# Performance work log

Measured on AMD Instinct MI355X. Metric: run time of the kernel, lower is better.

## Reference

```python
import jax, jax.numpy as jnp
import numpy as np

E = 768; H = 64; W = 64; K = 3; PAD = 1
CH = [30, 100, 150, 220, 268]


def _conv3x3(x, w, b):
    out = jax.lax.conv_general_dilated(x, w, (1, 1), ((PAD, PAD), (PAD, PAD)),
                                       dimension_numbers=('NCHW', 'OIHW', 'NCHW'))
    return out + b[None, :, None, None]


def _deform_conv(x, offset, mask, w, b):
    # modulated deform_conv2d, group=1, stride=1, dil=1, pad=1 (torchvision semantics)
    N, C, Hh, Ww = x.shape
    KK = K * K
    off = offset.reshape(N, KK, 2, Hh, Ww)  # [...,0]=dy, [...,1]=dx per kernel tap
    ky = jnp.repeat(jnp.arange(K), K).astype(x.dtype)
    kx = jnp.tile(jnp.arange(K), K).astype(x.dtype)
    hg = jnp.arange(Hh, dtype=x.dtype)[None, None, :, None]
    wg = jnp.arange(Ww, dtype=x.dtype)[None, None, None, :]
    py = hg - PAD + ky[None, :, None, None] + off[:, :, 0]  # [N,9,H,W]
    px = wg - PAD + kx[None, :, None, None] + off[:, :, 1]
    y0 = jnp.floor(py); x0 = jnp.floor(px)
    xf = x.reshape(N, C, Hh * Ww)

    def gather(yi, xi):
        valid = ((yi >= 0) & (yi <= Hh - 1) & (xi >= 0) & (xi <= Ww - 1)).astype(x.dtype)
        yc = jnp.clip(yi, 0, Hh - 1).astype(jnp.int32)
        xc = jnp.clip(xi, 0, Ww - 1).astype(jnp.int32)
        idx = (yc * Ww + xc).reshape(N, 1, KK * Hh * Ww)
        g = jnp.take_along_axis(xf, idx, axis=2).reshape(N, C, KK, Hh, Ww)
        return g * valid[:, None]

    wy1 = py - y0; wx1 = px - x0; wy0 = 1.0 - wy1; wx0 = 1.0 - wx1
    samp = (gather(y0, x0) * (wy0 * wx0)[:, None]
            + gather(y0, x0 + 1) * (wy0 * wx1)[:, None]
            + gather(y0 + 1, x0) * (wy1 * wx0)[:, None]
            + gather(y0 + 1, x0 + 1) * (wy1 * wx1)[:, None])
    samp = samp * mask[:, None]  # modulation
    out = jnp.einsum('nckhw,ock->nohw', samp, w.reshape(w.shape[0], C, KK))
    return out + b[None, :, None, None]


def _block(x, conv_w, conv_b, off_w, off_b, msk_w, msk_b, bn_g, bn_b):
    # DefConv2d.forward: conv -> offset/mask linears -> deform conv -> BN(train stats) -> relu
    N, C, Hh, Ww = x.shape
    om = _conv3x3(x, conv_w, conv_b)
    om_hwc = om.transpose(0, 2, 3, 1)
    offset = (om_hwc @ off_w.T + off_b).transpose(0, 3, 1, 2)  # [N,18,H,W]
    mask = jax.nn.softmax(om_hwc @ msk_w.T + msk_b, axis=-1)   # [N,H,W,9]
    mask = mask.reshape(N, K * K, Hh, Ww)  # raw reshape, exactly as torch .reshape (no permute)
    out = _deform_conv(x, offset, mask, conv_w, conv_b)
    mu = out.mean(axis=(0, 2, 3), keepdims=True)
    var = out.var(axis=(0, 2, 3), keepdims=True)
    out = (out - mu) / jnp.sqrt(var + 1e-5) * bn_g[None, :, None, None] + bn_b[None, :, None, None]
    return jax.nn.relu(out)


def _cam(x, chq_w, chv_w, chz_w, ln_g, ln_b, spq_w, spv_w):
    xin = x
    N, C, Hh, Ww = x.shape  # N must be 1 (matches torch reshapes)
    # channel attention
    wv = jnp.einsum('nchw,oc->nohw', x, chv_w).reshape(C // 2, Hh * Ww)
    wq = jax.nn.softmax(jnp.einsum('nchw,oc->nohw', x, chq_w).reshape(Hh * Ww))
    wz = chz_w @ (wv @ wq)  # [C]
    wz = (wz - wz.mean()) / jnp.sqrt(wz.var() + 1e-5) * ln_g + ln_b
    x = jax.nn.sigmoid(wz)[None, :, None, None] * x
    # spatial attention
    wq = jax.nn.softmax(jnp.einsum('nchw,oc->nohw', x, spq_w).max(axis=(2, 3)).reshape(C // 2))
    wv = jnp.einsum('nchw,oc->nohw', x, spv_w).reshape(C // 2, Hh * Ww)
    wz = jax.nn.sigmoid(wq @ wv).reshape(1, 1, Hh, Ww)
    return wz * x + xin


def _forward(x1, x2, x3, x4, x5, conv_w, conv_b, off_w, off_b, msk_w, msk_b, bn_g, bn_b,
             chq_w, chv_w, chz_w, ln_g, ln_b, spq_w, spv_w,
             w1, w2, w3a, w3b, w4a, w4b, w5a, w5b, norm_g, norm_b):
    xper = [t.transpose(0, 3, 1, 2) for t in (x1, x2, x3, x4, x5)]
    blk = lambda t: _block(t, conv_w, conv_b, off_w, off_b, msk_w, msk_b, bn_g, bn_b)
    c1 = lambda t, w: jnp.einsum('nchw,oc->nohw', t, w)
    o1 = c1(blk(xper[0]), w1)
    o2 = c1(blk(xper[1]), w2)
    o3 = c1(blk(xper[2]), w3a) + c1(xper[2], w3b)
    o4 = c1(blk(xper[3]), w4a) + c1(xper[3], w4b)
    o5 = c1(blk(xper[4]), w5a) + c1(xper[4], w5b)
    out = jnp.concatenate((o1, o2, o3, o4, o5), axis=1)  # sum(CH)=768 channels
    out = _cam(out, chq_w, chv_w, chz_w, ln_g, ln_b, spq_w, spv_w)
    out = (out + xper[4]).transpose(0, 2, 3, 1)
    mu = out.mean(-1, keepdims=True)
    var = out.var(-1, keepdims=True)
    return (out - mu) / jnp.sqrt(var + 1e-5) * norm_g + norm_b


def setup_inputs() -> dict:
    key = jax.random.key(0)
    ks = iter(jax.random.split(key, 40))
    rnd = lambda shape, s=0.05: jax.random.normal(next(ks), shape, dtype=jnp.float32) * s
    d = {}
    for i in range(5):
        d[f'x{i+1}'] = jax.random.normal(next(ks), (1, H, W, E), dtype=jnp.float32)
    d['conv_w'] = rnd((E, E, 3, 3), 0.02)
    d['conv_b'] = jnp.zeros((E,), jnp.float32)
    d['off_w'] = rnd((2 * 9, E), 0.01); d['off_b'] = jnp.zeros((18,), jnp.float32)
    d['msk_w'] = rnd((9, E), 0.01); d['msk_b'] = jnp.zeros((9,), jnp.float32)
    d['bn_g'] = jnp.ones((E,), jnp.float32); d['bn_b'] = jnp.zeros((E,), jnp.float32)
    C = sum(CH)  # 768
    d['chq_w'] = rnd((1, C)); d['chv_w'] = rnd((C // 2, C)); d['chz_w'] = rnd((C, C // 2))
    d['ln_g'] = jnp.ones((C,), jnp.float32); d['ln_b'] = jnp.zeros((C,), jnp.float32)
    d['spq_w'] = rnd((C // 2, C)); d['spv_w'] = rnd((C // 2, C))
    d['w1'] = rnd((CH[0], E)); d['w2'] = rnd((CH[1], E))
    d['w3a'] = rnd((CH[2], E)); d['w3b'] = rnd((CH[2], E))
    d['w4a'] = rnd((CH[3], E)); d['w4b'] = rnd((CH[3], E))
    d['w5a'] = rnd((CH[4], E)); d['w5b'] = rnd((CH[4], E))
    d['norm_g'] = jnp.ones((E,), jnp.float32); d['norm_b'] = jnp.zeros((E,), jnp.float32)
    return d


def reference(x1, x2, x3, x4, x5, conv_w, conv_b, off_w, off_b, msk_w, msk_b, bn_g, bn_b,
              chq_w, chv_w, chz_w, ln_g, ln_b, spq_w, spv_w,
              w1, w2, w3a, w3b, w4a, w4b, w5a, w5b, norm_g, norm_b):
    return _forward(x1, x2, x3, x4, x5, conv_w, conv_b, off_w, off_b, msk_w, msk_b, bn_g, bn_b,
                    chq_w, chv_w, chz_w, ln_g, ln_b, spq_w, spv_w,
                    w1, w2, w3a, w3b, w4a, w4b, w5a, w5b, norm_g, norm_b)
```

## Files before the change

### kernel.cpp

```cpp
#include <hip/hip_runtime.h>
#include <cstdint>
#include <cstddef>

#define HW 4096
#define CDIM 768
#define PPIX 4356

typedef unsigned short u16;
typedef __attribute__((ext_vector_type(8))) short short8;
typedef __attribute__((ext_vector_type(4))) float f32x4;

__device__ __forceinline__ float bf2f(u16 u) { return __uint_as_float(((unsigned)u) << 16); }
__device__ __forceinline__ u16 f2bf(float f) {
    unsigned u = __float_as_uint(f);
    unsigned r = (u + 0x7fffu + ((u >> 16) & 1u)) >> 16;
    return (u16)r;
}
__device__ __forceinline__ float lof(unsigned u) { return __uint_as_float(u << 16); }
__device__ __forceinline__ float hif(unsigned u) { return __uint_as_float(u & 0xffff0000u); }
__device__ __forceinline__ int swz(int r) { return ((r >> 1) ^ (r >> 3)) & 3; }

__device__ __forceinline__ void gl16(const u16* g, u16* l) {
    __builtin_amdgcn_global_load_lds(
        (const __attribute__((address_space(1))) unsigned int*)g,
        (__attribute__((address_space(3))) unsigned int*)l, 16, 0, 0);
}

enum GMode { G_CONV = 0, G_PROJ = 2, G_SPAT = 3 };

struct ProjP {
    const u16* b1[5];
    const u16* b2[5];
    int ch[5];
    int choff[5];
};

template <int MODE>
__launch_bounds__(256, 4)
__global__ void k_gemm128(const u16* __restrict__ xpad, const u16* __restrict__ blkA,
                          const u16* __restrict__ Wt, const float* __restrict__ bias,
                          u16* __restrict__ outb, float* __restrict__ outf, ProjP pp) {
    const int z = blockIdx.z;
    const int m0 = blockIdx.x * 128;
    const int n0 = blockIdx.y * 128;

    int Nrows, ntap, choff = 0, ldo = CDIM;
    const u16 *Az = nullptr, *Ac = nullptr, *B1 = nullptr, *B2 = nullptr;
    if constexpr (MODE == G_CONV) {
        Az = xpad + (size_t)z * PPIX * CDIM; B1 = Wt; Nrows = 768; ntap = 9;
    } else if constexpr (MODE == G_PROJ) {
        Ac = blkA + (size_t)z * HW * CDIM;
        Az = xpad + (size_t)z * PPIX * CDIM;
        B1 = pp.b1[z]; B2 = pp.b2[z];
        Nrows = pp.ch[z]; choff = pp.choff[z];
        ntap = B2 ? 2 : 1;
        if (n0 >= Nrows) return;
    } else {
        Ac = blkA; B1 = Wt; Nrows = 384; ntap = 1; ldo = 384;
    }

    __shared__ __align__(16) u16 As[128 * 32];
    __shared__ __align__(16) u16 Bs[128 * 32];

    const int t = threadIdx.x;
    const int lane = t & 63;
    const int wid = t >> 6;
    const int wrow = (wid >> 1) * 64, wcol = (wid & 1) * 64;
    const int lm = lane & 15;
    const int quad = lane >> 4;

    const int rS = t >> 2;
    const int cs0 = (t & 3) ^ swz(rS);
    const int cs1 = (t & 3) ^ swz(64 + rS);

    const u16 *a0 = nullptr, *a1 = nullptr, *a0x = nullptr, *a1x = nullptr;
    if constexpr (MODE == G_CONV) {
        int p0 = m0 + rS, p1 = m0 + 64 + rS;
        a0 = Az + (size_t)(((p0 >> 6)) * 66 + (p0 & 63)) * CDIM + cs0 * 8;
        a1 = Az + (size_t)(((p1 >> 6)) * 66 + (p1 & 63)) * CDIM + cs1 * 8;
    } else if constexpr (MODE == G_PROJ) {
        int p0 = m0 + rS, p1 = m0 + 64 + rS;
        a0 = Ac + (size_t)p0 * CDIM + cs0 * 8;
        a1 = Ac + (size_t)p1 * CDIM + cs1 * 8;
        a0x = Az + (size_t)(((p0 >> 6) + 1) * 66 + (p0 & 63) + 1) * CDIM + cs0 * 8;
        a1x = Az + (size_t)(((p1 >> 6) + 1) * 66 + (p1 & 63) + 1) * CDIM + cs1 * 8;
    } else {
        a0 = Ac + (size_t)(m0 + rS) * CDIM + cs0 * 8;
        a1 = Ac + (size_t)(m0 + 64 + rS) * CDIM + cs1 * 8;
    }
    const u16* b0 = B1 + (size_t)(n0 + rS) * CDIM + cs0 * 8;
    const u16* b1p = B1 + (size_t)(n0 + 64 + rS) * CDIM + cs1 * 8;
    const u16 *c0 = nullptr, *c1 = nullptr;
    if constexpr (MODE == G_PROJ) {
        if (B2) {
            c0 = B2 + (size_t)(n0 + rS) * CDIM + cs0 * 8;
            c1 = B2 + (size_t)(n0 + 64 + rS) * CDIM + cs1 * 8;
        }
    }

    u16* dA0 = &As[(0 * 4 + wid) * 512];
    u16* dA1 = &As[(1 * 4 + wid) * 512];
    u16* dB0 = &Bs[(0 * 4 + wid) * 512];
    u16* dB1 = &Bs[(1 * 4 + wid) * 512];

    f32x4 acc[4][4];
#pragma unroll
    for (int i = 0; i < 4; i++)
#pragma unroll
        for (int j = 0; j < 4; j++) acc[i][j] = (f32x4){0.f, 0.f, 0.f, 0.f};

    const int totS = ntap * 24;
    int tap = 0;
    int tA = 0, tB = 0, kO = 0;

    for (int s = 0; s < totS; ++s) {
        __syncthreads();
        if constexpr (MODE == G_CONV) {
            gl16(a0 + tA + kO, dA0);
            gl16(a1 + tA + kO, dA1);
            gl16(b0 + tB + kO, dB0);
            gl16(b1p + tB + kO, dB1);
        } else if constexpr (MODE == G_PROJ) {
            if (tap == 0) {
                gl16(a0 + kO, dA0);
                gl16(a1 + kO, dA1);
                gl16(b0 + kO, dB0);
                gl16(b1p + kO, dB1);
            } else {
                gl16(a0x + kO, dA0);
                gl16(a1x + kO, dA1);
                gl16(c0 + kO, dB0);
                gl16(c1 + kO, dB1);
            }
        } else {
            gl16(a0 + kO, dA0);
            gl16(a1 + kO, dA1);
            gl16(b0 + kO, dB0);
            gl16(b1p + kO, dB1);
        }
        __syncthreads();
        short8 af[4], bf[4];
#pragma unroll
        for (int i = 0; i < 4; i++) {
            int rr = wrow + i * 16 + lm;
            af[i] = *(const short8*)&As[rr * 32 + ((quad ^ swz(rr)) * 8)];
        }
#pragma unroll
        for (int j = 0; j < 4; j++) {
            int rr = wcol + j * 16 + lm;
            bf[j] = *(const short8*)&Bs[rr * 32 + ((quad ^ swz(rr)) * 8)];
        }
#pragma unroll
        for (int i = 0; i < 4; i++)
#pragma unroll
            for (int j = 0; j < 4; j++)
                acc[i][j] = __builtin_amdgcn_mfma_f32_16x16x32_bf16(af[i], bf[j], acc[i][j], 0, 0, 0);
        tap++;
        if constexpr (MODE == G_CONV) {
            tA += (tap == 3 || tap == 6) ? 64 * CDIM : CDIM;
            tB += CDIM * CDIM;
            if (tap == 9) { tap = 0; tA = 0; tB = 0; kO += 32; }
        } else {
            if (tap == ntap) { tap = 0; kO += 32; }
        }
    }

    if constexpr (MODE == G_CONV) {
        u16* outz = outb + (size_t)z * HW * CDIM;
#pragma unroll
        for (int j = 0; j < 4; j++) {
            int gc = n0 + wcol + j * 16 + lm;
            float bv = bias[gc];
#pragma unroll
            for (int i = 0; i < 4; i++)
#pragma unroll
                for (int r = 0; r < 4; r++) {
                    int gr = m0 + wrow + i * 16 + quad * 4 + r;
                    outz[(size_t)gr * CDIM + gc] = f2bf(acc[i][j][r] + bv);
                }
        }
    } else {
#pragma unroll
        for (int j = 0; j < 4; j++) {
            int gc = n0 + wcol + j * 16 + lm;
            if (gc < Nrows) {
#pragma unroll
                for (int i = 0; i < 4; i++)
#pragma unroll
                    for (int r = 0; r < 4; r++) {
                        int gr = m0 + wrow + i * 16 + quad * 4 + r;
                        outf[(size_t)gr * ldo + choff + gc] = acc[i][j][r];
                    }
            }
        }
    }
}

__launch_bounds__(512, 4)
__global__ void k_conv256(const u16* __restrict__ xpad, const u16* __restrict__ Wt,
                          const float* __restrict__ bias, u16* __restrict__ outb) {
    const int z = blockIdx.z;
    const int m0 = blockIdx.x * 128;
    const int n0 = blockIdx.y * 256;
    const u16* Az = xpad + (size_t)z * PPIX * CDIM;

    __shared__ __align__(16) u16 As[2][128 * 32];
    __shared__ __align__(16) u16 Bs[2][256 * 32];

    const int t = threadIdx.x;
    const int lane = t & 63;
    const int wid = t >> 6;
    const int wrow = (wid >> 2) * 64, wcol = (wid & 3) * 64;
    const int lm = lane & 15;
    const int quad = lane >> 4;

    const int rA = t >> 2;
    const int cA = (t & 3) ^ swz(rA);
    const int rB0 = t >> 2;
    const int cB0 = (t & 3) ^ swz(rB0);
    const int rB1 = 128 + (t >> 2);
    const int cB1 = (t & 3) ^ swz(rB1);

    const int p0 = m0 + rA;
    const u16* aB = Az + (size_t)((p0 >> 6) * 66 + (p0 & 63)) * CDIM + cA * 8;
    const u16* bB0 = Wt + (size_t)(n0 + rB0) * CDIM + cB0 * 8;
    const u16* bB1 = Wt + (size_t)(n0 + rB1) * CDIM + cB1 * 8;

    f32x4 acc[4][4];
#pragma unroll
    for (int i = 0; i < 4; i++)
#pragma unroll
        for (int j = 0; j < 4; j++) acc[i][j] = (f32x4){0.f, 0.f, 0.f, 0.f};

    gl16(aB, &As[0][wid * 512]);
    gl16(bB0, &Bs[0][wid * 512]);
    gl16(bB1, &Bs[0][4096 + wid * 512]);

    int tap = 0, tA = 0, tB = 0, kO = 0;

    for (int s = 0; s < 216; ++s) {
        const int cur = s & 1;
        const int nxt = cur ^ 1;
        __syncthreads();
        const bool hasN = (s + 1 < 216);
        if (hasN) {
            tap++;
            tA += (tap == 3 || tap == 6) ? 64 * CDIM : CDIM;
            tB += CDIM * CDIM;
            if (tap == 9) { tap = 0; tA = 0; tB = 0; kO += 32; }
            gl16(aB + tA + kO, &As[nxt][wid * 512]);
            gl16(bB0 + tB + kO, &Bs[nxt][wid * 512]);
            gl16(bB1 + tB + kO, &Bs[nxt][4096 + wid * 512]);
        }
        short8 af[4];
#pragma unroll
        for (int i = 0; i < 4; i++) {
            int rr = wrow + i * 16 + lm;
            af[i] = *(const short8*)&As[cur][rr * 32 + ((quad ^ swz(rr)) * 8)];
        }
#pragma unroll
        for (int j = 0; j < 4; j++) {
            int rr = wcol + j * 16 + lm;
            short8 bf = *(const short8*)&Bs[cur][rr * 32 + ((quad ^ swz(rr)) * 8)];
#pragma unroll
            for (int i = 0; i < 4; i++)
                acc[i][j] = __builtin_amdgcn_mfma_f32_16x16x32_bf16(af[i], bf, acc[i][j], 0, 0, 0);
        }
    }

    u16* outz = outb + (size_t)z * HW * CDIM;
#pragma unroll
    for (int j = 0; j < 4; j++) {
        int gc = n0 + wcol + j * 16 + lm;
        float bv = bias[gc];
#pragma unroll
        for (int i = 0; i < 4; i++)
#pragma unroll
            for (int r = 0; r < 4; r++) {
                int gr = m0 + wrow + i * 16 + quad * 4 + r;
                outz[(size_t)gr * CDIM + gc] = f2bf(acc[i][j][r] + bv);
            }
    }
}

__launch_bounds__(512, 4)
__global__ void k_gdef(const u16* __restrict__ xpad, const u16* __restrict__ Wt,
                       const int4* __restrict__ idx4, const float4* __restrict__ w4,
                       const float* __restrict__ bias, u16* __restrict__ outb) {
    const int z = blockIdx.z;
    const int m0 = blockIdx.x * 128;
    const int n0 = blockIdx.y * 256;
    const u16* Az = xpad + (size_t)z * PPIX * CDIM;
    const int4* idxz = idx4 + (size_t)z * 9 * 4096;
    const float4* w4z = w4 + (size_t)z * 9 * 4096;

    __shared__ __align__(16) u16 As[2][128 * 32];
    __shared__ __align__(16) u16 Bs[2][256 * 32];

    const int t = threadIdx.x;
    const int lane = t & 63;
    const int wid = t >> 6;
    const int wrow = (wid >> 2) * 64, wcol = (wid & 3) * 64;
    const int lm = lane & 15;
    const int quad = lane >> 4;

    const int rA = t >> 2;
    const int cA = (t & 3) ^ swz(rA);
    const int rB0 = t >> 2;
    const int cB0 = (t & 3) ^ swz(rB0);
    const int rB1 = 128 + (t >> 2);
    const int cB1 = (t & 3) ^ swz(rB1);

    f32x4 acc[4][4];
#pragma unroll
    for (int i = 0; i < 4; i++)
#pragma unroll
        for (int j = 0; j < 4; j++) acc[i][j] = (f32x4){0.f, 0.f, 0.f, 0.f};

    const u16* bP0;
    const u16* bP1;
    int dOff[4];
    float4 wv;

    auto setupSub = [&](int sn) {
        const u16* Bb = Wt + (size_t)sn * CDIM * CDIM;
        bP0 = Bb + (size_t)(n0 + rB0) * CDIM + cB0 * 8;
        bP1 = Bb + (size_t)(n0 + rB1) * CDIM + cB1 * 8;
        int4 iv = idxz[sn * 4096 + m0 + rA];
        wv = w4z[sn * 4096 + m0 + rA];
        dOff[0] = (iv.x + cA * 8) * 2;
        dOff[1] = (iv.y + cA * 8) * 2;
        dOff[2] = (iv.z + cA * 8) * 2;
        dOff[3] = (iv.w + cA * 8) * 2;
    };

    auto blend4 = [&](const uint4* L) -> uint4 {
        auto bl = [&](unsigned a, unsigned b, unsigned c2, unsigned d) -> unsigned {
            float lo = fmaf(wv.x, lof(a), fmaf(wv.y, lof(b), fmaf(wv.z, lof(c2), wv.w * lof(d))));
            float hi = fmaf(wv.x, hif(a), fmaf(wv.y, hif(b), fmaf(wv.z, hif(c2), wv.w * hif(d))));
            return __builtin_amdgcn_perm(__float_as_uint(hi), __float_as_uint(lo), 0x07060302u);
        };
        uint4 o;
        o.x = bl(L[0].x, L[1].x, L[2].x, L[3].x);
        o.y = bl(L[0].y, L[1].y, L[2].y, L[3].y);
        o.z = bl(L[0].z, L[1].z, L[2].z, L[3].z);
        o.w = bl(L[0].w, L[1].w, L[2].w, L[3].w);
        return o;
    };

    setupSub(0);
    int stagedSub = 0;

    {
        uint4 L[4];
#pragma unroll
        for (int k = 0; k < 4; k++)
            L[k] = *(const uint4*)((const char*)Az + dOff[k]);
        gl16(bP0, &Bs[0][wid * 512]);
        gl16(bP1, &Bs[0][4096 + wid * 512]);
        uint4 o = blend4(L);
        *(uint4*)&As[0][t * 8] = o;
    }

    for (int s = 0; s < 216; ++s) {
        const int cur = s & 1;
        const int nxt = cur ^ 1;
        __syncthreads();
        const bool hasN = (s + 1 < 216);
        uint4 L[4];
        if (hasN) {
            int kn = (s + 1) - stagedSub * 24;
            if (kn == 24) { setupSub(++stagedSub); kn = 0; }
            const int cb = kn * 64;
#pragma unroll
            for (int k = 0; k < 4; k++)
                L[k] = *(const uint4*)((const char*)Az + dOff[k] + cb);
            gl16(bP0 + kn * 32, &Bs[nxt][wid * 512]);
            gl16(bP1 + kn * 32, &Bs[nxt][4096 + wid * 512]);
        }
        short8 af[4];
#pragma unroll
        for (int i = 0; i < 4; i++) {
            int rr = wrow + i * 16 + lm;
            af[i] = *(const short8*)&As[cur][rr * 32 + ((quad ^ swz(rr)) * 8)];
        }
#pragma unroll
        for (int j = 0; j < 4; j++) {
            int rr = wcol + j * 16 + lm;
            short8 bf = *(const short8*)&Bs[cur][rr * 32 + ((quad ^ swz(rr)) * 8)];
#pragma unroll
            for (int i = 0; i < 4; i++)
                acc[i][j] = __builtin_amdgcn_mfma_f32_16x16x32_bf16(af[i], bf, acc[i][j], 0, 0, 0);
        }
        if (hasN) {
            uint4 o = blend4(L);
            *(uint4*)&As[nxt][t * 8] = o;
        }
    }

    u16* outz = outb + (size_t)z * HW * CDIM;
#pragma unroll
    for (int j = 0; j < 4; j++) {
        int gc = n0 + wcol + j * 16 + lm;
        float bv = bias[gc];
#pragma unroll
        for (int i = 0; i < 4; i++)
#pragma unroll
            for (int r = 0; r < 4; r++) {
                int gr = m0 + wrow + i * 16 + quad * 4 + r;
                outz[(size_t)gr * CDIM + gc] = f2bf(acc[i][j][r] + bv);
            }
    }
}

struct Ptr5 { const float* p[5]; };

__global__ void k_prep_xpad(Ptr5 xs, u16* __restrict__ xpad) {
    int z = blockIdx.y;
    int pidx = blockIdx.x;
    int ph = pidx / 66, pw = pidx - ph * 66;
    int e0 = threadIdx.x * 4;
    u16* d = xpad + ((size_t)z * PPIX + pidx) * CDIM + e0;
    if (ph == 0 || ph == 65 || pw == 0 || pw == 65) {
        *(uint2*)d = make_uint2(0, 0);
        return;
    }
    const float* s = xs.p[z] + ((size_t)((ph - 1) * 64 + (pw - 1))) * CDIM + e0;
    float4 v = *(const float4*)s;
    u16 o[4] = {f2bf(v.x), f2bf(v.y), f2bf(v.z), f2bf(v.w)};
    *(uint2*)d = *(uint2*)o;
}

__global__ void k_prep_wt(const float* __restrict__ cw, u16* __restrict__ Wt) {
    int o = blockIdx.x;
    for (int c = threadIdx.x; c < 768; c += 256) {
        const float* s = cw + ((size_t)o * 768 + c) * 9;
#pragma unroll
        for (int k = 0; k < 9; k++)
            Wt[(size_t)k * 768 * 768 + (size_t)o * 768 + c] = f2bf(s[k]);
    }
}

struct WbP { const float* src[9]; u16* dst[9]; int n[9]; };

__global__ void k_prep_wb(WbP wp) {
    int m = blockIdx.y;
    int i = (blockIdx.x * 256 + threadIdx.x) * 4;
    if (i >= wp.n[m]) return;
    float4 v = *(const float4*)(wp.src[m] + i);
    u16* d = wp.dst[m] + i;
    d[0] = f2bf(v.x); d[1] = f2bf(v.y); d[2] = f2bf(v.z); d[3] = f2bf(v.w);
}

__global__ void k_offmask1(const u16* __restrict__ om, const float* __restrict__ off_w,
                           const float* __restrict__ off_b, const float* __restrict__ msk_w,
                           const float* __restrict__ msk_b, float* __restrict__ offs,
                           float* __restrict__ msoft) {
    int z = blockIdx.y;
    int wid = threadIdx.x >> 6, lane = threadIdx.x & 63;
    int p = blockIdx.x * 4 + wid;
    const u16* r = om + (size_t)z * HW * CDIM + (size_t)p * CDIM;
    float v[12];
#pragma unroll
    for (int j = 0; j < 12; j++) v[j] = bf2f(r[lane + 64 * j]);
    float lg[9];
#pragma unroll
    for (int qq = 0; qq < 27; qq++) {
        const float* wr = (qq < 18) ? (off_w + qq * 768) : (msk_w + (qq - 18) * 768);
        float s = 0.f;
#pragma unroll
        for (int j = 0; j < 12; j++) s += v[j] * wr[lane + 64 * j];
#pragma unroll
        for (int o = 32; o > 0; o >>= 1) s += __shfl_xor(s, o, 64);
        if (qq < 18) {
            if (lane == qq) offs[((size_t)z * HW + p) * 18 + qq] = s + off_b[qq];
        } else {
            lg[qq - 18] = s + msk_b[qq - 18];
        }
    }
    float mx = -1e30f;
#pragma unroll
    for (int j = 0; j < 9; j++) mx = fmaxf(mx, lg[j]);
    float sum = 0.f;
#pragma unroll
    for (int j = 0; j < 9; j++) { lg[j] = expf(lg[j] - mx); sum += lg[j]; }
    float inv = 1.f / sum;
#pragma unroll
    for (int j = 0; j < 9; j++)
        if (lane == j) msoft[(size_t)z * 36864 + p * 9 + j] = lg[j] * inv;
}

__device__ __forceinline__ int cidx(int y, int x) {
    int yc = min(max(y, 0), 63), xc = min(max(x, 0), 63);
    return ((yc + 1) * 66 + (xc + 1)) * CDIM;
}
__device__ __forceinline__ float cval(int y, int x) {
    return (y >= 0 && y < 64 && x >= 0 && x < 64) ? 1.f : 0.f;
}

__global__ void k_offmask2(const float* __restrict__ offs, const float* __restrict__ msoft,
                           int4* __restrict__ idx4o, float4* __restrict__ w4o) {
    int id = blockIdx.x * 256 + threadIdx.x;
    int z = id / 36864, r = id % 36864, k = r >> 12, p = r & 4095;
    const float* ofz = offs + ((size_t)z * HW + p) * 18;
    float dy = ofz[2 * k], dx = ofz[2 * k + 1];
    float mk = msoft[(size_t)z * 36864 + k * 4096 + p];
    int h = p >> 6, w = p & 63;
    float py = (float)(h - 1 + k / 3) + dy;
    float px = (float)(w - 1 + k % 3) + dx;
    float y0f = floorf(py), x0f = floorf(px);
    int y0 = (int)y0f, x0 = (int)x0f;
    float wy1 = py - y0f, wx1 = px - x0f, wy0 = 1.f - wy1, wx0 = 1.f - wx1;
    idx4o[id] = make_int4(cidx(y0, x0), cidx(y0, x0 + 1), cidx(y0 + 1, x0), cidx(y0 + 1, x0 + 1));
    w4o[id] = make_float4(wy0 * wx0 * cval(y0, x0) * mk, wy0 * wx1 * cval(y0, x0 + 1) * mk,
                          wy1 * wx0 * cval(y0 + 1, x0) * mk, wy1 * wx1 * cval(y0 + 1, x0 + 1) * mk);
}

__global__ void k_bnstats2(const u16* __restrict__ dout, float* __restrict__ pb1,
                           float* __restrict__ pb2) {
    const int z = blockIdx.z, seg = blockIdx.y;
    const int cx = threadIdx.x & 7, py = threadIdx.x >> 3;
    const int c0 = blockIdx.x * 64 + cx * 8;
    const u16* base = dout + (size_t)z * HW * CDIM + (size_t)(seg * 1024) * CDIM + c0;
    float s1[8] = {0.f, 0.f, 0.f, 0.f, 0.f, 0.f, 0.f, 0.f};
    float s2[8] = {0.f, 0.f, 0.f, 0.f, 0.f, 0.f, 0.f, 0.f};
    for (int p = py; p < 1024; p += 32) {
        uint4 v = *(const uint4*)(base + (size_t)p * CDIM);
        const u16* u = (const u16*)&v;
#pragma unroll
        for (int e = 0; e < 8; e++) {
            float f = bf2f(u[e]);
            s1[e] += f; s2[e] += f * f;
        }
    }
    __shared__ float l1[32][64], l2[32][64];
#pragma unroll
    for (int e = 0; e < 8; e++) {
        l1[py][cx * 8 + e] = s1[e];
        l2[py][cx * 8 + e] = s2[e];
    }
    __syncthreads();
    if (threadIdx.x < 64) {
        float a = 0.f, b = 0.f;
        for (int y = 0; y < 32; y++) { a += l1[y][threadIdx.x]; b += l2[y][threadIdx.x]; }
        int ch = blockIdx.x * 64 + threadIdx.x;
        pb1[(z * 4 + seg) * 768 + ch] = a;
        pb2[(z * 4 + seg) * 768 + ch] = b;
    }
}

__global__ void k_bnfinal(const float* __restrict__ pb1, const float* __restrict__ pb2,
                          float* __restrict__ mu, float* __restrict__ rs) {
    int i = blockIdx.x * 256 + threadIdx.x;
    if (i >= 3840) return;
    int z = i / 768, ch = i % 768;
    float a = 0.f, b = 0.f;
#pragma unroll
    for (int s = 0; s < 4; s++) {
        a += pb1[(z * 4 + s) * 768 + ch];
        b += pb2[(z * 4 + s) * 768 + ch];
    }
    float m = a / 4096.f;
    float var = b / 4096.f - m * m;
    mu[i] = m;
    rs[i] = rsqrtf(var + 1e-5f);
}

__global__ void k_bnapply(const u16* __restrict__ dout, const float* __restrict__ mu,
                          const float* __restrict__ rs, const float* __restrict__ g,
                          const float* __restrict__ b, u16* __restrict__ blk) {
    size_t i = ((size_t)blockIdx.x * 256 + threadIdx.x) * 8;
    int c = (int)(i % CDIM);
    int z = (int)(i / ((size_t)HW * CDIM));
    const float* muz = mu + z * 768;
    const float* rsz = rs + z * 768;
    uint4 in = *(const uint4*)(dout + i);
    const u16* u = (const u16*)&in;
    u16 o[8];
#pragma unroll
    for (int e = 0; e < 8; e++) {
        int ce = c + e;
        float v = (bf2f(u[e]) - muz[ce]) * rsz[ce] * g[ce] + b[ce];
        o[e] = f2bf(fmaxf(v, 0.f));
    }
    *(uint4*)(blk + i) = *(uint4*)o;
}

__global__ void k_q(const float* __restrict__ X, const float* __restrict__ chq,
                    float* __restrict__ q) {
    int wid = threadIdx.x >> 6, lane = threadIdx.x & 63;
    int p = blockIdx.x * 4 + wid;
    const float* xr = X + (size_t)p * CDIM;
    float s = 0.f;
#pragma unroll
    for (int j = 0; j < 12; j++) s += xr[lane + 64 * j] * chq[lane + 64 * j];
#pragma unroll
    for (int o = 32; o > 0; o >>= 1) s += __shfl_xor(s, o, 64);
    if (lane == 0) q[p] = s;
}

__global__ void k_soft4096(const float* __restrict__ q, float* __restrict__ sqn,
                           float* __restrict__ xq) {
    __shared__ float red[4];
    int tid = threadIdx.x, lane = tid & 63, wid = tid >> 6;
    float m = -1e30f;
    for (int i = tid; i < 4096; i += 256) m = fmaxf(m, q[i]);
    for (int o = 32; o > 0; o >>= 1) m = fmaxf(m, __shfl_xor(m, o, 64));
    if (lane == 0) red[wid] = m;
    __syncthreads();
    float bm = fmaxf(fmaxf(red[0], red[1]), fmaxf(red[2], red[3]));
    __syncthreads();
    float s = 0.f;
    for (int i = tid; i < 4096; i += 256) {
        float e = expf(q[i] - bm);
        sqn[i] = e; s += e;
    }
    for (int o = 32; o > 0; o >>= 1) s += __shfl_xor(s, o, 64);
    if (lane == 0) red[wid] = s;
    __syncthreads();
    float inv = 1.f / (red[0] + red[1] + red[2] + red[3]);
    for (int i = tid; i < 4096; i += 256) sqn[i] *= inv;
    for (int c = tid; c < 768; c += 256) xq[c] = 0.f;
}

__global__ void k_xq(const float* __restrict__ X, const float* __restrict__ sqn,
                     float* __restrict__ xq) {
    int p0 = blockIdx.x * 128;
    for (int c = threadIdx.x; c < 768; c += 256) {
        float a = 0.f;
        for (int p = p0; p < p0 + 128; p++) a += sqn[p] * X[(size_t)p * CDIM + c];
        atomicAdd(&xq[c], a);
    }
}

__global__ void k_gemv384(const float* __restrict__ chv, const float* __restrict__ xq,
                          float* __restrict__ wvq) {
    int wid = threadIdx.x >> 6, lane = threadIdx.x & 63;
    int o = blockIdx.x * 4 + wid;
    const float* r = chv + (size_t)o * 768;
    float s = 0.f;
#pragma unroll
    for (int j = 0; j < 12; j++) s += r[lane + 64 * j] * xq[lane + 64 * j];
#pragma unroll
    for (int off = 32; off > 0; off >>= 1) s += __shfl_xor(s, off, 64);
    if (lane == 0) wvq[o] = s;
}

__global__ void k_gemv768(const float* __restrict__ chz, const float* __restrict__ wvq,
                          float* __restrict__ wzv) {
    int wid = threadIdx.x >> 6, lane = threadIdx.x & 63;
    int c = blockIdx.x * 4 + wid;
    const float* r = chz + (size_t)c * 384;
    float s = 0.f;
#pragma unroll
    for (int j = 0; j < 6; j++) s += r[lane + 64 * j] * wvq[lane + 64 * j];
#pragma unroll
    for (int off = 32; off > 0; off >>= 1) s += __shfl_xor(s, off, 64);
    if (lane == 0) wzv[c] = s;
}

__global__ void k_lngate(const float* __restrict__ wzv, const float* __restrict__ lng,
                         const float* __restrict__ lnb, float* __restrict__ sgate) {
    __shared__ float red[8];
    int tid = threadIdx.x, lane = tid & 63, wid = tid >> 6;
    float a = wzv[tid], b = wzv[tid + 256], c = wzv[tid + 512];
    float s1 = a + b + c, s2 = a * a + b * b + c * c;
    for (int o = 32; o > 0; o >>= 1) { s1 += __shfl_xor(s1, o, 64); s2 += __shfl_xor(s2, o, 64); }
    if (lane == 0) { red[wid] = s1; red[4 + wid] = s2; }
    __syncthreads();
    s1 = red[0] + red[1] + red[2] + red[3];
    s2 = red[4] + red[5] + red[6] + red[7];
    float mean = s1 / 768.f, var = s2 / 768.f - mean * mean, rstd = rsqrtf(var + 1e-5f);
    for (int cc = tid; cc < 768; cc += 256) {
        float tv = (wzv[cc] - mean) * rstd * lng[cc] + lnb[cc];
        sgate[cc] = 1.f / (1.f + expf(-tv));
    }
}

__global__ void k_xatt(const float* __restrict__ X, const float* __restrict__ sgate,
                       u16* __restrict__ xatt) {
    size_t i = ((size_t)blockIdx.x * 256 + threadIdx.x) * 4;
    int c = (int)(i % CDIM);
    float4 v = *(const float4*)(X + i);
    u16 o[4] = {f2bf(v.x * sgate[c]), f2bf(v.y * sgate[c + 1]),
                f2bf(v.z * sgate[c + 2]), f2bf(v.w * sgate[c + 3])};
    *(uint2*)(xatt + i) = *(uint2*)o;
}

__global__ void k_colmax24(const float* __restrict__ P2, float* __restrict__ m2) {
    __shared__ float red[16][17];
    int col = blockIdx.x * 16 + threadIdx.x;
    float m = -1e30f;
    for (int p = threadIdx.y; p < 4096; p += 16) m = fmaxf(m, P2[(size_t)p * 384 + col]);
    red[threadIdx.y][threadIdx.x] = m;
    __syncthreads();
    if (threadIdx.y == 0) {
        for (int y = 1; y < 16; y++) m = fmaxf(m, red[y][threadIdx.x]);
        m2[col] = m;
    }
}

__global__ void k_sm384(const float* __restrict__ m2, float* __restrict__ sq2) {
    __shared__ float red[6];
    int tid = threadIdx.x, lane = tid & 63, wid = tid >> 6;
    float v = m2[tid];
    float m = v;
    for (int o = 32; o > 0; o >>= 1) m = fmaxf(m, __shfl_xor(m, o, 64));
    if (lane == 0) red[wid] = m;
    __syncthreads();
    m = red[0];
    for (int w = 1; w < 6; w++) m = fmaxf(m, red[w]);
    __syncthreads();
    float e = expf(v - m);
    float s = e;
    for (int o = 32; o > 0; o >>= 1) s += __shfl_xor(s, o, 64);
    if (lane == 0) red[wid] = s;
    __syncthreads();
    float tot = 0.f;
    for (int w = 0; w < 6; w++) tot += red[w];
    sq2[tid] = e / tot;
}

__global__ void k_sv(const float* __restrict__ sq2, const float* __restrict__ spv,
                     float* __restrict__ sv) {
    __shared__ float part[4][64];
    int c = blockIdx.x * 64 + (threadIdx.x & 63);
    int seg = threadIdx.x >> 6;
    float a = 0.f;
    for (int o = seg * 96; o < seg * 96 + 96; o++) a += sq2[o] * spv[(size_t)o * 768 + c];
    part[seg][threadIdx.x & 63] = a;
    __syncthreads();
    if (seg == 0) sv[c] = part[0][threadIdx.x] + part[1][threadIdx.x] +
                          part[2][threadIdx.x] + part[3][threadIdx.x];
}

__global__ void k_final(const float* __restrict__ X, const float* __restrict__ x5,
                        const float* __restrict__ sgate, const float* __restrict__ sv,
                        const float* __restrict__ ng, const float* __restrict__ nb,
                        float* __restrict__ out) {
    int wid = threadIdx.x >> 6, lane = threadIdx.x & 63;
    int p = blockIdx.x * 4 + wid;
    const float* xr = X + (size_t)p * CDIM;
    const float* x5r = x5 + (size_t)p * CDIM;
    float xa[12];
    float d = 0.f;
#pragma unroll
    for (int j = 0; j < 12; j++) {
        int c = lane + 64 * j;
        float a = xr[c] * sgate[c];
        xa[j] = a;
        d += sv[c] * a;
    }
#pragma unroll
    for (int o = 32; o > 0; o >>= 1) d += __shfl_xor(d, o, 64);
    float wz2 = 1.f / (1.f + expf(-d));
    float s1 = 0.f, s2 = 0.f;
#pragma unroll
    for (int j = 0; j < 12; j++) {
        int c = lane + 64 * j;
        float y = wz2 * xa[j] + xr[c] + x5r[c];
        xa[j] = y;
        s1 += y; s2 += y * y;
    }
#pragma unroll
    for (int o = 32; o > 0; o >>= 1) { s1 += __shfl_xor(s1, o, 64); s2 += __shfl_xor(s2, o, 64); }
    float mean = s1 / 768.f, var = s2 / 768.f - mean * mean, rstd = rsqrtf(var + 1e-5f);
#pragma unroll
    for (int j = 0; j < 12; j++) {
        int c = lane + 64 * j;
        out[(size_t)p * CDIM + c] = (xa[j] - mean) * rstd * ng[c] + nb[c];
    }
}

extern "C" void kernel_launch(void* const* d_in, const int* in_sizes, int n_in,
                              void* d_out, int out_size, void* d_ws, size_t ws_size,
                              hipStream_t stream) {
    const float* xin[5];
    for (int i = 0; i < 5; i++) xin[i] = (const float*)d_in[i];
    const float* conv_w = (const float*)d_in[5];
    const float* conv_b = (const float*)d_in[6];
    const float* off_w = (const float*)d_in[7];
    const float* off_b = (const float*)d_in[8];
    const float* msk_w = (const float*)d_in[9];
    const float* msk_b = (const float*)d_in[10];
    const float* bn_g = (const float*)d_in[11];
    const float* bn_b = (const float*)d_in[12];
    const float* chq_w = (const float*)d_in[13];
    const float* chv_w = (const float*)d_in[14];
    const float* chz_w = (const float*)d_in[15];
    const float* ln_g = (const float*)d_in[16];
    const float* ln_b = (const float*)d_in[17];
    const float* spq_w = (const float*)d_in[18];
    const float* spv_w = (const float*)d_in[19];
    const float* wsrc[8];
    for (int i = 0; i < 8; i++) wsrc[i] = (const float*)d_in[20 + i];
    const float* norm_g = (const float*)d_in[28];
    const float* norm_b = (const float*)d_in[29];
    float* out = (float*)d_out;

    char* wsb = (char*)d_ws;
    size_t off = 0;
    auto take = [&](size_t n) -> char* {
        char* p = wsb + off;
        off = (off + n + 255) & ~(size_t)255;
        return p;
    };
    u16* xpad = (u16*)take(5ll * PPIX * CDIM * 2);
    u16* Wt = (u16*)take(9ll * CDIM * CDIM * 2);
    u16* omblk = (u16*)take(5ll * HW * CDIM * 2);
    float* offs = (float*)take(5ll * HW * 18 * 4);
    float* msoft = (float*)take(5ll * 36864 * 4);
    int4* idx4 = (int4*)take(5ll * 9 * 4096 * 16);
    float4* w4 = (float4*)take(5ll * 9 * 4096 * 16);
    u16* dout = (u16*)take(5ll * HW * CDIM * 2);
    u16* wb = (u16*)take(1790ll * 768 * 2);
    float* Xcat = (float*)take((size_t)HW * CDIM * 4);
    float* mu = (float*)take(5 * 768 * 4);
    float* rs = (float*)take(5 * 768 * 4);
    float* pb1 = (float*)take(5 * 4 * 768 * 4);
    float* pb2 = (float*)take(5 * 4 * 768 * 4);
    float* qv = (float*)take(4096 * 4);
    float* sqn = (float*)take(4096 * 4);
    float* xq = (float*)take(768 * 4);
    float* wvq = (float*)take(384 * 4);
    float* wzv = (float*)take(768 * 4);
    float* sgate = (float*)take(768 * 4);
    float* m2 = (float*)take(384 * 4);
    float* sq2 = (float*)take(384 * 4);
    float* sv = (float*)take(768 * 4);
    u16* xatt = dout;
    float* P2 = (float*)((char*)dout + 8388608);
    u16* blk = omblk;
    (void)ws_size; (void)in_sizes; (void)n_in; (void)out_size;

    int rows[9] = {30, 100, 150, 150, 220, 220, 268, 268, 384};
    int roff[9]; int acc = 0;
    for (int i = 0; i < 9; i++) { roff[i] = acc; acc += rows[i]; }
    u16* spqb = wb + (size_t)roff[8] * 768;

    WbP wp;
    for (int i = 0; i < 8; i++) { wp.src[i] = wsrc[i]; wp.dst[i] = wb + (size_t)roff[i] * 768; wp.n[i] = rows[i] * 768; }
    wp.src[8] = spq_w; wp.dst[8] = spqb; wp.n[8] = rows[8] * 768;

    ProjP pp;
    pp.b1[0] = wb + (size_t)roff[0] * 768; pp.b2[0] = nullptr;
    pp.b1[1] = wb + (size_t)roff[1] * 768; pp.b2[1] = nullptr;
    pp.b1[2] = wb + (size_t)roff[2] * 768; pp.b2[2] = wb + (size_t)roff[3] * 768;
    pp.b1[3] = wb + (size_t)roff[4] * 768; pp.b2[3] = wb + (size_t)roff[5] * 768;
    pp.b1[4] = wb + (size_t)roff[6] * 768; pp.b2[4] = wb + (size_t)roff[7] * 768;
    int chs[5] = {30, 100, 150, 220, 268};
    int cof[5] = {0, 30, 130, 280, 500};
    for (int i = 0; i < 5; i++) { pp.ch[i] = chs[i]; pp.choff[i] = cof[i]; }
    ProjP pdum = {};

    Ptr5 xs;
    for (int i = 0; i < 5; i++) xs.p[i] = xin[i];

    k_prep_xpad<<<dim3(PPIX, 5), 192, 0, stream>>>(xs, xpad);
    k_prep_wt<<<dim3(768), 256, 0, stream>>>(conv_w, Wt);
    k_prep_wb<<<dim3(288, 9), 256, 0, stream>>>(wp);

    k_conv256<<<dim3(32, 3, 5), 512, 0, stream>>>(xpad, Wt, conv_b, omblk);
    k_offmask1<<<dim3(1024, 5), 256, 0, stream>>>(omblk, off_w, off_b, msk_w, msk_b, offs, msoft);
    k_offmask2<<<dim3(720), 256, 0, stream>>>(offs, msoft, idx4, w4);
    k_gdef<<<dim3(32, 3, 5), 512, 0, stream>>>(xpad, Wt, idx4, w4, conv_b, dout);
    k_bnstats2<<<dim3(12, 4, 5), 256, 0, stream>>>(dout, pb1, pb2);
    k_bnfinal<<<dim3(15), 256, 0, stream>>>(pb1, pb2, mu, rs);
    k_bnapply<<<dim3(7680), 256, 0, stream>>>(dout, mu, rs, bn_g, bn_b, blk);
    k_gemm128<G_PROJ><<<dim3(32, 3, 5), 256, 0, stream>>>(xpad, blk, nullptr, nullptr,
                                                          nullptr, Xcat, pp);

    k_q<<<dim3(1024), 256, 0, stream>>>(Xcat, chq_w, qv);
    k_soft4096<<<dim3(1), 256, 0, stream>>>(qv, sqn, xq);
    k_xq<<<dim3(32), 256, 0, stream>>>(Xcat, sqn, xq);
    k_gemv384<<<dim3(96), 256, 0, stream>>>(chv_w, xq, wvq);
    k_gemv768<<<dim3(192), 256, 0, stream>>>(chz_w, wvq, wzv);
    k_lngate<<<dim3(1), 256, 0, stream>>>(wzv, ln_g, ln_b, sgate);
    k_xatt<<<dim3(3072), 256, 0, stream>>>(Xcat, sgate, xatt);
    k_gemm128<G_SPAT><<<dim3(32, 3, 1), 256, 0, stream>>>(xpad, xatt, spqb, nullptr,
                                                          nullptr, P2, pdum);
    k_colmax24<<<dim3(24), dim3(16, 16), 0, stream>>>(P2, m2);
    k_sm384<<<dim3(1), 384, 0, stream>>>(m2, sq2);
    k_sv<<<dim3(12), 256, 0, stream>>>(sq2, spv_w, sv);

    k_final<<<dim3(1024), 256, 0, stream>>>(Xcat, xin[4], sgate, sv, norm_g, norm_b, out);
}
```

Before: 996.3 us.

## Split deform GEMM K dimension across two halves and batch offmask pixels

The deformable-conv GEMM now splits its 216-step K loop into two halves run by separate blocks, doubling the grid from 480 to 960 blocks. Each half writes fp32 partial sums that the BN stats and apply kernels add together. Separately, the offset/mask projection kernel gives each wave four pixels, so each weight load is reused four times. The split adds 2x fp32 output traffic (about 126MB written and read twice) in exchange for better occupancy on the big GEMM.

```diff
diff --git a/kernel.cpp b/kernel.cpp
--- a/kernel.cpp
+++ b/kernel.cpp
@@ -286,10 +286,14 @@
 __launch_bounds__(512, 4)
 __global__ void k_gdef(const u16* __restrict__ xpad, const u16* __restrict__ Wt,
                        const int4* __restrict__ idx4, const float4* __restrict__ w4,
-                       const float* __restrict__ bias, u16* __restrict__ outb) {
+                       const float* __restrict__ bias, float* __restrict__ ph0,
+                       float* __restrict__ ph1) {
     const int z = blockIdx.z;
-    const int m0 = blockIdx.x * 128;
+    const int half = blockIdx.x >> 5;
+    const int m0 = (blockIdx.x & 31) * 128;
     const int n0 = blockIdx.y * 256;
+    const int kB = half * 768;
+    const int kE = half * 384;
     const u16* Az = xpad + (size_t)z * PPIX * CDIM;
     const int4* idxz = idx4 + (size_t)z * 9 * 4096;
     const float4* w4z = w4 + (size_t)z * 9 * 4096;
@@ -355,28 +359,28 @@
         uint4 L[4];
 #pragma unroll
         for (int k = 0; k < 4; k++)
-            L[k] = *(const uint4*)((const char*)Az + dOff[k]);
-        gl16(bP0, &Bs[0][wid * 512]);
-        gl16(bP1, &Bs[0][4096 + wid * 512]);
+            L[k] = *(const uint4*)((const char*)Az + dOff[k] + kB);
+        gl16(bP0 + kE, &Bs[0][wid * 512]);
+        gl16(bP1 + kE, &Bs[0][4096 + wid * 512]);
         uint4 o = blend4(L);
         *(uint4*)&As[0][t * 8] = o;
     }
 
-    for (int s = 0; s < 216; ++s) {
+    for (int s = 0; s < 108; ++s) {
         const int cur = s & 1;
         const int nxt = cur ^ 1;
         __syncthreads();
-        const bool hasN = (s + 1 < 216);
+        const bool hasN = (s + 1 < 108);
         uint4 L[4];
         if (hasN) {
-            int kn = (s + 1) - stagedSub * 24;
-            if (kn == 24) { setupSub(++stagedSub); kn = 0; }
-            const int cb = kn * 64;
+            int kn = (s + 1) - stagedSub * 12;
+            if (kn == 12) { setupSub(++stagedSub); kn = 0; }
+            const int cb = kB + kn * 64;
 #pragma unroll
             for (int k = 0; k < 4; k++)
                 L[k] = *(const uint4*)((const char*)Az + dOff[k] + cb);
-            gl16(bP0 + kn * 32, &Bs[nxt][wid * 512]);
-            gl16(bP1 + kn * 32, &Bs[nxt][4096 + wid * 512]);
+            gl16(bP0 + kE + kn * 32, &Bs[nxt][wid * 512]);
+            gl16(bP1 + kE + kn * 32, &Bs[nxt][4096 + wid * 512]);
         }
         short8 af[4];
 #pragma unroll
@@ -398,17 +402,17 @@
         }
     }
 
-    u16* outz = outb + (size_t)z * HW * CDIM;
+    float* outz = (half ? ph1 : ph0) + (size_t)z * HW * CDIM;
 #pragma unroll
     for (int j = 0; j < 4; j++) {
         int gc = n0 + wcol + j * 16 + lm;
-        float bv = bias[gc];
+        float bv = half ? 0.f : bias[gc];
 #pragma unroll
         for (int i = 0; i < 4; i++)
 #pragma unroll
             for (int r = 0; r < 4; r++) {
                 int gr = m0 + wrow + i * 16 + quad * 4 + r;
-                outz[(size_t)gr * CDIM + gc] = f2bf(acc[i][j][r] + bv);
+                outz[(size_t)gr * CDIM + gc] = acc[i][j][r] + bv;
             }
     }
 }
@@ -458,36 +462,52 @@
                            float* __restrict__ msoft) {
     int z = blockIdx.y;
     int wid = threadIdx.x >> 6, lane = threadIdx.x & 63;
-    int p = blockIdx.x * 4 + wid;
-    const u16* r = om + (size_t)z * HW * CDIM + (size_t)p * CDIM;
-    float v[12];
-#pragma unroll
-    for (int j = 0; j < 12; j++) v[j] = bf2f(r[lane + 64 * j]);
-    float lg[9];
-#pragma unroll
+    int p0 = blockIdx.x * 16 + wid * 4;
+    const u16* rbase = om + (size_t)z * HW * CDIM + (size_t)p0 * CDIM;
+    float v[4][12];
+#pragma unroll
+    for (int pp = 0; pp < 4; pp++)
+#pragma unroll
+        for (int j = 0; j < 12; j++) v[pp][j] = bf2f(rbase[pp * CDIM + lane + 64 * j]);
+    float lg[4][9];
     for (int qq = 0; qq < 27; qq++) {
         const float* wr = (qq < 18) ? (off_w + qq * 768) : (msk_w + (qq - 18) * 768);
-        float s = 0.f;
-#pragma unroll
-        for (int j = 0; j < 12; j++) s += v[j] * wr[lane + 64 * j];
-#pragma unroll
-        for (int o = 32; o > 0; o >>= 1) s += __shfl_xor(s, o, 64);
+        float w[12];
+#pragma unroll
+        for (int j = 0; j < 12; j++) w[j] = wr[lane + 64 * j];
+        float s[4] = {0.f, 0.f, 0.f, 0.f};
+#pragma unroll
+        for (int pp = 0; pp < 4; pp++)
+#pragma unroll
+            for (int j = 0; j < 12; j++) s[pp] = fmaf(v[pp][j], w[j], s[pp]);
+#pragma unroll
+        for (int pp = 0; pp < 4; pp++)
+#pragma unroll
+            for (int o = 32; o > 0; o >>= 1) s[pp] += __shfl_xor(s[pp], o, 64);
         if (qq < 18) {
-            if (lane == qq) offs[((size_t)z * HW + p) * 18 + qq] = s + off_b[qq];
+            if (lane == qq) {
+#pragma unroll
+                for (int pp = 0; pp < 4; pp++)
+                    offs[((size_t)z * HW + p0 + pp) * 18 + qq] = s[pp] + off_b[qq];
+            }
         } else {
-            lg[qq - 18] = s + msk_b[qq - 18];
-        }
-    }
-    float mx = -1e30f;
-#pragma unroll
-    for (int j = 0; j < 9; j++) mx = fmaxf(mx, lg[j]);
-    float sum = 0.f;
-#pragma unroll
-    for (int j = 0; j < 9; j++) { lg[j] = expf(lg[j] - mx); sum += lg[j]; }
-    float inv = 1.f / sum;
-#pragma unroll
-    for (int j = 0; j < 9; j++)
-        if (lane == j) msoft[(size_t)z * 36864 + p * 9 + j] = lg[j] * inv;
+#pragma unroll
+            for (int pp = 0; pp < 4; pp++) lg[pp][qq - 18] = s[pp] + msk_b[qq - 18];
+        }
+    }
+#pragma unroll
+    for (int pp = 0; pp < 4; pp++) {
+        float mx = -1e30f;
+#pragma unroll
+        for (int j = 0; j < 9; j++) mx = fmaxf(mx, lg[pp][j]);
+        float sum = 0.f;
+#pragma unroll
+        for (int j = 0; j < 9; j++) { lg[pp][j] = expf(lg[pp][j] - mx); sum += lg[pp][j]; }
+        float inv = 1.f / sum;
+#pragma unroll
+        for (int j = 0; j < 9; j++)
+            if (lane == j) msoft[(size_t)z * 36864 + (p0 + pp) * 9 + j] = lg[pp][j] * inv;
+    }
 }
 
 __device__ __forceinline__ int cidx(int y, int x) {
@@ -516,22 +536,24 @@
                           wy1 * wx0 * cval(y0 + 1, x0) * mk, wy1 * wx1 * cval(y0 + 1, x0 + 1) * mk);
 }
 
-__global__ void k_bnstats2(const u16* __restrict__ dout, float* __restrict__ pb1,
-                           float* __restrict__ pb2) {
+__global__ void k_bnstats2(const float* __restrict__ ph0, const float* __restrict__ ph1,
+                           float* __restrict__ pb1, float* __restrict__ pb2) {
     const int z = blockIdx.z, seg = blockIdx.y;
     const int cx = threadIdx.x & 7, py = threadIdx.x >> 3;
     const int c0 = blockIdx.x * 64 + cx * 8;
-    const u16* base = dout + (size_t)z * HW * CDIM + (size_t)(seg * 1024) * CDIM + c0;
+    const float* b0 = ph0 + ((size_t)z * HW + seg * 1024) * CDIM + c0;
+    const float* b1 = ph1 + ((size_t)z * HW + seg * 1024) * CDIM + c0;
     float s1[8] = {0.f, 0.f, 0.f, 0.f, 0.f, 0.f, 0.f, 0.f};
     float s2[8] = {0.f, 0.f, 0.f, 0.f, 0.f, 0.f, 0.f, 0.f};
     for (int p = py; p < 1024; p += 32) {
-        uint4 v = *(const uint4*)(base + (size_t)p * CDIM);
-        const u16* u = (const u16*)&v;
-#pragma unroll
-        for (int e = 0; e < 8; e++) {
-            float f = bf2f(u[e]);
-            s1[e] += f; s2[e] += f * f;
-        }
+        float4 x0 = *(const float4*)(b0 + (size_t)p * CDIM);
+        float4 x1 = *(const float4*)(b0 + (size_t)p * CDIM + 4);
+        float4 y0 = *(const float4*)(b1 + (size_t)p * CDIM);
+        float4 y1 = *(const float4*)(b1 + (size_t)p * CDIM + 4);
+        float f[8] = {x0.x + y0.x, x0.y + y0.y, x0.z + y0.z, x0.w + y0.w,
+                      x1.x + y1.x, x1.y + y1.y, x1.z + y1.z, x1.w + y1.w};
+#pragma unroll
+        for (int e = 0; e < 8; e++) { s1[e] += f[e]; s2[e] += f[e] * f[e]; }
     }
     __shared__ float l1[32][64], l2[32][64];
 #pragma unroll
@@ -566,21 +588,26 @@
     rs[i] = rsqrtf(var + 1e-5f);
 }
 
-__global__ void k_bnapply(const u16* __restrict__ dout, const float* __restrict__ mu,
-                          const float* __restrict__ rs, const float* __restrict__ g,
-                          const float* __restrict__ b, u16* __restrict__ blk) {
+__global__ void k_bnapply(const float* __restrict__ ph0, const float* __restrict__ ph1,
+                          const float* __restrict__ mu, const float* __restrict__ rs,
+                          const float* __restrict__ g, const float* __restrict__ b,
+                          u16* __restrict__ blk) {
     size_t i = ((size_t)blockIdx.x * 256 + threadIdx.x) * 8;
     int c = (int)(i % CDIM);
     int z = (int)(i / ((size_t)HW * CDIM));
     const float* muz = mu + z * 768;
     const float* rsz = rs + z * 768;
-    uint4 in = *(const uint4*)(dout + i);
-    const u16* u = (const u16*)&in;
+    float4 x0 = *(const float4*)(ph0 + i);
+    float4 x1 = *(const float4*)(ph0 + i + 4);
+    float4 y0 = *(const float4*)(ph1 + i);
+    float4 y1 = *(const float4*)(ph1 + i + 4);
+    float f[8] = {x0.x + y0.x, x0.y + y0.y, x0.z + y0.z, x0.w + y0.w,
+                  x1.x + y1.x, x1.y + y1.y, x1.z + y1.z, x1.w + y1.w};
     u16 o[8];
 #pragma unroll
     for (int e = 0; e < 8; e++) {
         int ce = c + e;
-        float v = (bf2f(u[e]) - muz[ce]) * rsz[ce] * g[ce] + b[ce];
+        float v = (f[e] - muz[ce]) * rsz[ce] * g[ce] + b[ce];
         o[e] = f2bf(fmaxf(v, 0.f));
     }
     *(uint4*)(blk + i) = *(uint4*)o;
@@ -813,6 +840,8 @@
     int4* idx4 = (int4*)take(5ll * 9 * 4096 * 16);
     float4* w4 = (float4*)take(5ll * 9 * 4096 * 16);
     u16* dout = (u16*)take(5ll * HW * CDIM * 2);
+    float* ph0 = (float*)take(5ll * HW * CDIM * 4);
+    float* ph1 = (float*)take(5ll * HW * CDIM * 4);
     u16* wb = (u16*)take(1790ll * 768 * 2);
     float* Xcat = (float*)take((size_t)HW * CDIM * 4);
     float* mu = (float*)take(5 * 768 * 4);
@@ -861,12 +890,12 @@
     k_prep_wb<<<dim3(288, 9), 256, 0, stream>>>(wp);
 
     k_conv256<<<dim3(32, 3, 5), 512, 0, stream>>>(xpad, Wt, conv_b, omblk);
-    k_offmask1<<<dim3(1024, 5), 256, 0, stream>>>(omblk, off_w, off_b, msk_w, msk_b, offs, msoft);
+    k_offmask1<<<dim3(256, 5), 256, 0, stream>>>(omblk, off_w, off_b, msk_w, msk_b, offs, msoft);
     k_offmask2<<<dim3(720), 256, 0, stream>>>(offs, msoft, idx4, w4);
-    k_gdef<<<dim3(32, 3, 5), 512, 0, stream>>>(xpad, Wt, idx4, w4, conv_b, dout);
-    k_bnstats2<<<dim3(12, 4, 5), 256, 0, stream>>>(dout, pb1, pb2);
+    k_gdef<<<dim3(64, 3, 5), 512, 0, stream>>>(xpad, Wt, idx4, w4, conv_b, ph0, ph1);
+    k_bnstats2<<<dim3(12, 4, 5), 256, 0, stream>>>(ph0, ph1, pb1, pb2);
     k_bnfinal<<<dim3(15), 256, 0, stream>>>(pb1, pb2, mu, rs);
-    k_bnapply<<<dim3(7680), 256, 0, stream>>>(dout, mu, rs, bn_g, bn_b, blk);
+    k_bnapply<<<dim3(7680), 256, 0, stream>>>(ph0, ph1, mu, rs, bn_g, bn_b, blk);
     k_gemm128<G_PROJ><<<dim3(32, 3, 5), 256, 0, stream>>>(xpad, blk, nullptr, nullptr,
                                                           nullptr, Xcat, pp);
 
```

Measured after the change: 1.006 ms. No clear change (+1.0%).

## Remap conv/deform GEMM blocks per XCD and batch four pixels in offmask

Applied to the files above, without the earlier changes.

The conv and deformable-conv GEMM kernels now use a 1-D grid of 480 blocks. A decode maps each block id so that consecutive work tiles (same image, same weight columns) land on the same XCD, which should improve L2 reuse of the A and B tiles. The offset/mask projection kernel now has each wave handle four pixels, loading each weight row once and reusing it across the four dot products. This cuts weight reloads but raises register pressure and reduces the block count.

```diff
diff --git a/kernel.cpp b/kernel.cpp
--- a/kernel.cpp
+++ b/kernel.cpp
@@ -196,12 +196,19 @@
     }
 }
 
+__device__ __forceinline__ void xcd_decode(int bid, int& m0, int& n0, int& z) {
+    int work = (bid & 7) * 60 + (bid >> 3);
+    z = work / 96;
+    int rem = work - z * 96;
+    n0 = (rem >> 5) * 256;
+    m0 = (rem & 31) * 128;
+}
+
 __launch_bounds__(512, 4)
 __global__ void k_conv256(const u16* __restrict__ xpad, const u16* __restrict__ Wt,
                           const float* __restrict__ bias, u16* __restrict__ outb) {
-    const int z = blockIdx.z;
-    const int m0 = blockIdx.x * 128;
-    const int n0 = blockIdx.y * 256;
+    int m0, n0, z;
+    xcd_decode(blockIdx.x, m0, n0, z);
     const u16* Az = xpad + (size_t)z * PPIX * CDIM;
 
     __shared__ __align__(16) u16 As[2][128 * 32];
@@ -287,9 +294,8 @@
 __global__ void k_gdef(const u16* __restrict__ xpad, const u16* __restrict__ Wt,
                        const int4* __restrict__ idx4, const float4* __restrict__ w4,
                        const float* __restrict__ bias, u16* __restrict__ outb) {
-    const int z = blockIdx.z;
-    const int m0 = blockIdx.x * 128;
-    const int n0 = blockIdx.y * 256;
+    int m0, n0, z;
+    xcd_decode(blockIdx.x, m0, n0, z);
     const u16* Az = xpad + (size_t)z * PPIX * CDIM;
     const int4* idxz = idx4 + (size_t)z * 9 * 4096;
     const float4* w4z = w4 + (size_t)z * 9 * 4096;
@@ -458,36 +464,52 @@
                            float* __restrict__ msoft) {
     int z = blockIdx.y;
     int wid = threadIdx.x >> 6, lane = threadIdx.x & 63;
-    int p = blockIdx.x * 4 + wid;
-    const u16* r = om + (size_t)z * HW * CDIM + (size_t)p * CDIM;
-    float v[12];
-#pragma unroll
-    for (int j = 0; j < 12; j++) v[j] = bf2f(r[lane + 64 * j]);
-    float lg[9];
-#pragma unroll
+    int p0 = blockIdx.x * 16 + wid * 4;
+    const u16* rbase = om + (size_t)z * HW * CDIM + (size_t)p0 * CDIM;
+    float v[4][12];
+#pragma unroll
+    for (int pp = 0; pp < 4; pp++)
+#pragma unroll
+        for (int j = 0; j < 12; j++) v[pp][j] = bf2f(rbase[pp * CDIM + lane + 64 * j]);
+    float lg[4][9];
     for (int qq = 0; qq < 27; qq++) {
         const float* wr = (qq < 18) ? (off_w + qq * 768) : (msk_w + (qq - 18) * 768);
-        float s = 0.f;
-#pragma unroll
-        for (int j = 0; j < 12; j++) s += v[j] * wr[lane + 64 * j];
-#pragma unroll
-        for (int o = 32; o > 0; o >>= 1) s += __shfl_xor(s, o, 64);
+        float w[12];
+#pragma unroll
+        for (int j = 0; j < 12; j++) w[j] = wr[lane + 64 * j];
+        float s[4] = {0.f, 0.f, 0.f, 0.f};
+#pragma unroll
+        for (int pp = 0; pp < 4; pp++)
+#pragma unroll
+            for (int j = 0; j < 12; j++) s[pp] = fmaf(v[pp][j], w[j], s[pp]);
+#pragma unroll
+        for (int pp = 0; pp < 4; pp++)
+#pragma unroll
+            for (int o = 32; o > 0; o >>= 1) s[pp] += __shfl_xor(s[pp], o, 64);
         if (qq < 18) {
-            if (lane == qq) offs[((size_t)z * HW + p) * 18 + qq] = s + off_b[qq];
+            if (lane == qq) {
+#pragma unroll
+                for (int pp = 0; pp < 4; pp++)
+                    offs[((size_t)z * HW + p0 + pp) * 18 + qq] = s[pp] + off_b[qq];
+            }
         } else {
-            lg[qq - 18] = s + msk_b[qq - 18];
-        }
-    }
-    float mx = -1e30f;
-#pragma unroll
-    for (int j = 0; j < 9; j++) mx = fmaxf(mx, lg[j]);
-    float sum = 0.f;
-#pragma unroll
-    for (int j = 0; j < 9; j++) { lg[j] = expf(lg[j] - mx); sum += lg[j]; }
-    float inv = 1.f / sum;
-#pragma unroll
-    for (int j = 0; j < 9; j++)
-        if (lane == j) msoft[(size_t)z * 36864 + p * 9 + j] = lg[j] * inv;
+#pragma unroll
+            for (int pp = 0; pp < 4; pp++) lg[pp][qq - 18] = s[pp] + msk_b[qq - 18];
+        }
+    }
+#pragma unroll
+    for (int pp = 0; pp < 4; pp++) {
+        float mx = -1e30f;
+#pragma unroll
+        for (int j = 0; j < 9; j++) mx = fmaxf(mx, lg[pp][j]);
+        float sum = 0.f;
+#pragma unroll
+        for (int j = 0; j < 9; j++) { lg[pp][j] = expf(lg[pp][j] - mx); sum += lg[pp][j]; }
+        float inv = 1.f / sum;
+#pragma unroll
+        for (int j = 0; j < 9; j++)
+            if (lane == j) msoft[(size_t)z * 36864 + (p0 + pp) * 9 + j] = lg[pp][j] * inv;
+    }
 }
 
 __device__ __forceinline__ int cidx(int y, int x) {
@@ -860,10 +882,10 @@
     k_prep_wt<<<dim3(768), 256, 0, stream>>>(conv_w, Wt);
     k_prep_wb<<<dim3(288, 9), 256, 0, stream>>>(wp);
 
-    k_conv256<<<dim3(32, 3, 5), 512, 0, stream>>>(xpad, Wt, conv_b, omblk);
-    k_offmask1<<<dim3(1024, 5), 256, 0, stream>>>(omblk, off_w, off_b, msk_w, msk_b, offs, msoft);
+    k_conv256<<<dim3(480), 512, 0, stream>>>(xpad, Wt, conv_b, omblk);
+    k_offmask1<<<dim3(256, 5), 256, 0, stream>>>(omblk, off_w, off_b, msk_w, msk_b, offs, msoft);
     k_offmask2<<<dim3(720), 256, 0, stream>>>(offs, msoft, idx4, w4);
-    k_gdef<<<dim3(32, 3, 5), 512, 0, stream>>>(xpad, Wt, idx4, w4, conv_b, dout);
+    k_gdef<<<dim3(480), 512, 0, stream>>>(xpad, Wt, idx4, w4, conv_b, dout);
     k_bnstats2<<<dim3(12, 4, 5), 256, 0, stream>>>(dout, pb1, pb2);
     k_bnfinal<<<dim3(15), 256, 0, stream>>>(pb1, pb2, mu, rs);
     k_bnapply<<<dim3(7680), 256, 0, stream>>>(dout, mu, rs, bn_g, bn_b, blk);
```

Measured after the change: 982.2 us. About the same (-1.4%).
